# Kernel optimization log

Hardware: AMD Instinct MI355X
Metric: run time of the kernel (lower is better)

Reference implementation:

```python
import jax, jax.numpy as jnp
import numpy as np

SENSOR_H, SENSOR_W = 256, 256
SPP = 16
BATCH, C, H_IMG, W_IMG = 4, 3, 1024, 1024


def setup_inputs() -> dict:
    key = jax.random.key(0)
    k1, k2 = jax.random.split(key)
    img = jax.random.uniform(k1, (BATCH, C, H_IMG, W_IMG), dtype=jnp.float32)
    jitter = jax.random.uniform(k2, (SPP, SENSOR_H, SENSOR_W, 2), dtype=jnp.float32)
    t = jnp.ones((1,), jnp.float32)
    return {"img": img, "t": t, "jitter": jitter}


def deform(pos, t):
    # Analytic per-axis foveation diffeomorphism [-1,1]^2 -> [-1,1]^2:
    #   f(u) = tanh(t*u)/tanh(t), f'(u) = t*(1 - tanh(t*u)^2)/tanh(t)
    # Jacobian is diagonal, so det = f'(x) * f'(y).
    tt = t[0]
    s = jnp.tanh(tt)
    th = jnp.tanh(tt * pos)
    warped = th / s                      # (..., 2)
    dd = tt * (1.0 - th * th) / s        # diagonal Jacobian entries (..., 2)
    det = dd[..., 0] * dd[..., 1]        # (...)
    return warped, det


def grid_sample_border(img, grid):
    # img: (b,c,H,W); grid: (spp,h,w,2) in [-1,1]
    # bilinear, padding_mode='border', align_corners=False (matches F.grid_sample)
    b, c, H, W = img.shape
    gx = (grid[..., 0] + 1.0) * (W / 2.0) - 0.5
    gy = (grid[..., 1] + 1.0) * (H / 2.0) - 0.5
    gx = jnp.clip(gx, 0.0, W - 1.0)
    gy = jnp.clip(gy, 0.0, H - 1.0)
    x0 = jnp.floor(gx)
    y0 = jnp.floor(gy)
    wx = (gx - x0)[None, None]           # (1,1,spp,h,w)
    wy = (gy - y0)[None, None]
    x0i = jnp.clip(x0.astype(jnp.int32), 0, W - 1)
    y0i = jnp.clip(y0.astype(jnp.int32), 0, H - 1)
    x1i = jnp.clip(x0i + 1, 0, W - 1)
    y1i = jnp.clip(y0i + 1, 0, H - 1)
    # fancy-index gather: result (b,c,spp,h,w); avoids tiling img over (b*spp)
    v00 = img[:, :, y0i, x0i]
    v01 = img[:, :, y0i, x1i]
    v10 = img[:, :, y1i, x0i]
    v11 = img[:, :, y1i, x1i]
    return (v00 * (1 - wx) * (1 - wy) + v01 * wx * (1 - wy)
            + v10 * (1 - wx) * wy + v11 * wx * wy)


def reference(img, t, jitter):
    step_x = 2.0 / SENSOR_W
    step_y = 2.0 / SENSOR_H
    px = jnp.arange(-1.0, 1.0, step_x, dtype=jnp.float32)
    py = jnp.arange(-1.0, 1.0, step_y, dtype=jnp.float32)
    gx, gy = jnp.meshgrid(px, py, indexing='xy')          # (h, w)
    pixel_pos = jnp.stack((gx, gy), axis=-1)[None]        # (1, h, w, 2)
    jit = jitter * jnp.array([step_x, step_y], jnp.float32)
    pos = pixel_pos + jit                                 # (spp, h, w, 2)
    warped, det = deform(pos, t)                          # (spp,h,w,2), (spp,h,w)
    samples = grid_sample_border(img, warped)             # (b, c, spp, h, w)
    weighted = jnp.mean(samples * det[None, None], axis=2)  # (b, c, h, w)
    area = jnp.mean(det, axis=0)[None, None]              # (1, 1, h, w)
    return weighted / area
```

## Files before the change

### kernel.cpp

```cpp
#include <hip/hip_runtime.h>

#define SPP   16
#define SH    256
#define SW    256
#define HI    1024
#define WI    1024
#define CH    3
#define BATCH 4

__device__ __forceinline__ float fast_tanh(float x) {
    const float e = __expf(2.0f * x);
    return (e - 1.0f) * __builtin_amdgcn_rcpf(e + 1.0f);
}

__global__ __launch_bounds__(256, 6) void foveated_split(
    const float* __restrict__ img,
    const float* __restrict__ t_ptr,
    const float* __restrict__ jitter,
    float* __restrict__ out)
{
    const int L   = (blockIdx.x & 7) * 1024 + (blockIdx.x >> 3);
    const int bh  = L & 1;
    const int grp = L >> 1;

    const int th  = threadIdx.x;
    const int sp  = th & 15;
    const int lpx = (th >> 4) & 3;
    const int wv  = th >> 6;
    const int pix = grp * 16 + wv * 4 + lpx;
    const int sx  = pix & (SW - 1);
    const int sy  = pix >> 8;

    const float step  = 2.0f / 256.0f;
    const float tt    = t_ptr[0];
    const float inv_s = __builtin_amdgcn_rcpf(fast_tanh(tt));

    const float2 j = ((const float2*)jitter)[sp * (SH * SW) + pix];
    const float posx = (-1.0f + sx * step) + j.x * step;
    const float posy = (-1.0f + sy * step) + j.y * step;

    const float thx = fast_tanh(tt * posx);
    const float thy = fast_tanh(tt * posy);
    const float ddx = tt * (1.0f - thx * thx) * inv_s;
    const float ddy = tt * (1.0f - thy * thy) * inv_s;
    const float det = ddx * ddy;

    float gx = (thx * inv_s + 1.0f) * (WI * 0.5f) - 0.5f;
    float gy = (thy * inv_s + 1.0f) * (HI * 0.5f) - 0.5f;
    gx = fminf(fmaxf(gx, 0.0f), (float)(WI - 1));
    gy = fminf(fmaxf(gy, 0.0f), (float)(HI - 1));

    const int xb = min((int)gx, WI - 2);
    const int yb = min((int)gy, HI - 2);
    const float fx = gx - (float)xb;
    const float fy = gy - (float)yb;

    const float w00 = (1.0f - fx) * (1.0f - fy) * det;
    const float w01 = fx * (1.0f - fy) * det;
    const float w10 = (1.0f - fx) * fy * det;
    const float w11 = fx * fy * det;

    const int i0 = yb * WI + xb;
    const int i1 = i0 + WI;
    const size_t plane = (size_t)HI * WI;

    const float* __restrict__ pb = img + (size_t)(bh * 6) * plane;
    float2 r0[6], r1[6];
    #pragma unroll
    for (int p = 0; p < 6; ++p) {
        r0[p] = *(const float2*)(pb + p * plane + i0);
        r1[p] = *(const float2*)(pb + p * plane + i1);
    }

    float acc[6];
    #pragma unroll
    for (int p = 0; p < 6; ++p)
        acc[p] = r0[p].x * w00 + r0[p].y * w01 + r1[p].x * w10 + r1[p].y * w11;

    float dsum = det;
    #pragma unroll
    for (int m = 1; m < 16; m <<= 1) {
        #pragma unroll
        for (int p = 0; p < 6; ++p)
            acc[p] += __shfl_xor(acc[p], m);
        dsum += __shfl_xor(dsum, m);
    }

    if (sp == 0) {
        const float inv_d = 1.0f / dsum;
        #pragma unroll
        for (int p = 0; p < 6; ++p)
            out[(size_t)(bh * 6 + p) * (SH * SW) + pix] = acc[p] * inv_d;
    }
}

extern "C" void kernel_launch(void* const* d_in, const int* in_sizes, int n_in,
                              void* d_out, int out_size, void* d_ws, size_t ws_size,
                              hipStream_t stream) {
    const float* img    = (const float*)d_in[0];
    const float* t      = (const float*)d_in[1];
    const float* jitter = (const float*)d_in[2];
    float* out          = (float*)d_out;

    hipLaunchKernelGGL(foveated_split, dim3(8192), dim3(256), 0, stream,
                       img, t, jitter, out);
}
```

Measured before the change: 114.4 us.

## Repack image to fp16 NHWC4 and gather all batches per sample

```diff
diff --git a/kernel.cpp b/kernel.cpp
--- a/kernel.cpp
+++ b/kernel.cpp
@@ -1,4 +1,5 @@
 #include <hip/hip_runtime.h>
+#include <hip/hip_fp16.h>
 
 #define SPP   16
 #define SH    256
@@ -8,9 +9,114 @@
 #define CH    3
 #define BATCH 4
 
+struct __attribute__((packed, aligned(8))) U4 { uint4 v; };
+
 __device__ __forceinline__ float fast_tanh(float x) {
     const float e = __expf(2.0f * x);
     return (e - 1.0f) * __builtin_amdgcn_rcpf(e + 1.0f);
+}
+
+__global__ __launch_bounds__(256) void repack_kernel(
+    const float* __restrict__ img, __half* __restrict__ dst)
+{
+    const int tid = blockIdx.x * 256 + threadIdx.x;
+    const int b   = tid >> 20;
+    const int pix = tid & (HI * WI - 1);
+    const float* p = img + (size_t)b * (CH * HI * WI) + pix;
+    union { __half2 h[2]; uint2 u; } v;
+    v.h[0] = __floats2half2_rn(p[0], p[HI * WI]);
+    v.h[1] = __floats2half2_rn(p[2 * HI * WI], 0.0f);
+    *(uint2*)(dst + ((size_t)tid << 2)) = v.u;
+}
+
+__global__ __launch_bounds__(256, 6) void foveated_nhwc_b(
+    const __half* __restrict__ pk,
+    const float* __restrict__ t_ptr,
+    const float* __restrict__ jitter,
+    float* __restrict__ out)
+{
+    const int L   = (blockIdx.x & 7) * 512 + (blockIdx.x >> 3);
+    const int th  = threadIdx.x;
+    const int sp  = th & 15;
+    const int lpx = th >> 4;
+    const int pix = L * 16 + lpx;
+    const int sx  = pix & (SW - 1);
+    const int sy  = pix >> 8;
+
+    const float step  = 2.0f / 256.0f;
+    const float tt    = t_ptr[0];
+    const float inv_s = __builtin_amdgcn_rcpf(fast_tanh(tt));
+
+    const float2 j = ((const float2*)jitter)[sp * (SH * SW) + pix];
+    const float posx = (-1.0f + sx * step) + j.x * step;
+    const float posy = (-1.0f + sy * step) + j.y * step;
+
+    const float thx = fast_tanh(tt * posx);
+    const float thy = fast_tanh(tt * posy);
+    const float ddx = tt * (1.0f - thx * thx) * inv_s;
+    const float ddy = tt * (1.0f - thy * thy) * inv_s;
+    const float det = ddx * ddy;
+
+    float gx = (thx * inv_s + 1.0f) * (WI * 0.5f) - 0.5f;
+    float gy = (thy * inv_s + 1.0f) * (HI * 0.5f) - 0.5f;
+    gx = fminf(fmaxf(gx, 0.0f), (float)(WI - 1));
+    gy = fminf(fmaxf(gy, 0.0f), (float)(HI - 1));
+
+    const int xb = min((int)gx, WI - 2);
+    const int yb = min((int)gy, HI - 2);
+    const float fx = gx - (float)xb;
+    const float fy = gy - (float)yb;
+
+    const __half2 W00 = __float2half2_rn((1.0f - fx) * (1.0f - fy) * det);
+    const __half2 W01 = __float2half2_rn(fx * (1.0f - fy) * det);
+    const __half2 W10 = __float2half2_rn((1.0f - fx) * fy * det);
+    const __half2 W11 = __float2half2_rn(fx * fy * det);
+
+    const int i0 = (yb * WI + xb) << 2;
+    const int i1 = i0 + (WI << 2);
+
+    uint4 r0[BATCH], r1[BATCH];
+    #pragma unroll
+    for (int b = 0; b < BATCH; ++b) {
+        const __half* pb = pk + (size_t)b * (HI * WI * 4);
+        r0[b] = ((const U4*)(pb + i0))->v;
+        r1[b] = ((const U4*)(pb + i1))->v;
+    }
+
+    float acc[BATCH * CH];
+    #pragma unroll
+    for (int b = 0; b < BATCH; ++b) {
+        const __half2* a = (const __half2*)&r0[b];
+        const __half2* c = (const __half2*)&r1[b];
+        __half2 sA = __hmul2(a[0], W00);
+        __half2 sB = __hmul2(a[1], W00);
+        sA = __hfma2(a[2], W01, sA);
+        sB = __hfma2(a[3], W01, sB);
+        sA = __hfma2(c[0], W10, sA);
+        sB = __hfma2(c[1], W10, sB);
+        sA = __hfma2(c[2], W11, sA);
+        sB = __hfma2(c[3], W11, sB);
+        const float2 fA = __half22float2(sA);
+        acc[b * CH + 0] = fA.x;
+        acc[b * CH + 1] = fA.y;
+        acc[b * CH + 2] = __low2float(sB);
+    }
+
+    float dsum = det;
+    #pragma unroll
+    for (int m = 1; m < 16; m <<= 1) {
+        #pragma unroll
+        for (int p = 0; p < BATCH * CH; ++p)
+            acc[p] += __shfl_xor(acc[p], m);
+        dsum += __shfl_xor(dsum, m);
+    }
+
+    if (sp == 0) {
+        const float inv_d = 1.0f / dsum;
+        #pragma unroll
+        for (int p = 0; p < BATCH * CH; ++p)
+            out[(size_t)p * (SH * SW) + pix] = acc[p] * inv_d;
+    }
 }
 
 __global__ __launch_bounds__(256, 6) void foveated_split(
@@ -102,6 +208,15 @@
     const float* jitter = (const float*)d_in[2];
     float* out          = (float*)d_out;
 
-    hipLaunchKernelGGL(foveated_split, dim3(8192), dim3(256), 0, stream,
-                       img, t, jitter, out);
-}
+    const size_t need = (size_t)BATCH * HI * WI * 4 * sizeof(__half);
+    if (ws_size >= need) {
+        __half* pkimg = (__half*)d_ws;
+        hipLaunchKernelGGL(repack_kernel, dim3(BATCH * HI * WI / 256), dim3(256),
+                           0, stream, img, pkimg);
+        hipLaunchKernelGGL(foveated_nhwc_b, dim3(4096), dim3(256), 0, stream,
+                           pkimg, t, jitter, out);
+    } else {
+        hipLaunchKernelGGL(foveated_split, dim3(8192), dim3(256), 0, stream,
+                           img, t, jitter, out);
+    }
+}
```

New measurement: 110.6 us. 3.3% less time.
